# Optimization experiments

Hardware: AMD Instinct MI355X
Metric: run time of the kernel (lower is better)

Reference implementation:

```python
import jax, jax.numpy as jnp
import numpy as np

NUM_MODES = 13   # 8192x8192 weight, mode_base=2, z-order-grouped pairs -> 13 modes of size 4
RANK = 8
MODE = 4
NUM_BASIS = 32
OUT_F = 8192
IN_F = 8192


def setup_inputs() -> dict:
    key = jax.random.key(0)
    k1, k2, k3 = jax.random.split(key, 3)
    basis_weights = jnp.clip(jax.random.normal(k1, (NUM_MODES, NUM_BASIS), jnp.float32), -3.0, 3.0)
    basis = jax.random.normal(k2, (NUM_BASIS, RANK, MODE, RANK), jnp.float32)
    rank_adapters = jax.random.uniform(k3, (NUM_MODES, RANK), jnp.float32, 0.5, 1.5)
    return {"basis_weights": basis_weights, "basis": basis, "rank_adapters": rank_adapters}


def _chain(cores):
    # cores: list of (r, m, r) tensors; returns chained (r, m^len, r)
    T = cores[0]
    for G in cores[1:]:
        T = jnp.einsum('aib,bjc->aijc', T, G).reshape(RANK, -1, RANK)
    return T


def reference(basis_weights, basis, rank_adapters):
    # decompress_cores: small GEMM over the shared basis, then rank-adapter scaling ('linear' act)
    cores = (basis_weights @ basis.reshape(NUM_BASIS, -1)).reshape(NUM_MODES, RANK, MODE, RANK)
    cores = cores * rank_adapters[:, :, None, None]
    core_list = [cores[m] for m in range(NUM_MODES)]
    # tensor-ring contraction with trace; split chain in half to bound intermediate memory
    half = NUM_MODES // 2
    L = _chain(core_list[:half])    # (r, MODE^6, r)
    R = _chain(core_list[half:])    # (r, MODE^7, r)
    w = jnp.einsum('aib,bja->ij', L, R).reshape((MODE,) * NUM_MODES)
    # inverse z-order reshape: each mode-4 dim = (row-bit, col-bit) interleaved pair
    w = w.reshape((2,) * (2 * NUM_MODES))
    perm = tuple(range(0, 2 * NUM_MODES, 2)) + tuple(range(1, 2 * NUM_MODES, 2))
    w = jnp.transpose(w, perm).reshape(OUT_F, IN_F)
    return w
```

## Files before the change

### kernel.cpp

```cpp
#include <hip/hip_runtime.h>


using bf16x8 = __attribute__((ext_vector_type(8))) short;
using f32x4  = __attribute__((ext_vector_type(4))) float;
using f32x16 = __attribute__((ext_vector_type(16))) float;

#define WS_LA    4096
#define WS_LB    20480
#define WS_RA    24576
#define WS_RB    40960
#define BOFF_AHI 262144
#define BOFF_ALO 786432
#define BOFF_BHI 1310720
#define BOFF_BLO 3407872

__device__ __forceinline__ unsigned short f2bf(float x) {
    unsigned int u = __builtin_bit_cast(unsigned int, x);
    u += 0x7fffu + ((u >> 16) & 1u);
    return (unsigned short)(u >> 16);
}
__device__ __forceinline__ float bf2f(unsigned short b) {
    unsigned int u = ((unsigned int)b) << 16;
    return __builtin_bit_cast(float, u);
}

__global__ void k_chains(const float* __restrict__ bw,
                         const float* __restrict__ basis,
                         const float* __restrict__ ra,
                         float* __restrict__ ws) {
    __shared__ float sCores[13 * 256];
    __shared__ float buf0[4096];
    __shared__ float buf1[4096];
    const int tid   = threadIdx.x;
    const int chain = blockIdx.x;

    const int s0   = (chain == 0) ? 0 : (chain == 1) ? 4 : (chain == 2) ? 6 : 10;
    const int nm   = (chain == 0) ? 4 : (chain == 1) ? 2 : (chain == 2) ? 4 : 3;
    const int wout = (chain == 0) ? WS_LA : (chain == 1) ? WS_LB
                   : (chain == 2) ? WS_RA : WS_RB;

    for (int e = tid; e < 13 * 256; e += 256) {
        int m    = e >> 8;
        int r1   = (e >> 5) & 7;
        int rest = e & 255;
        float s = 0.f;
#pragma unroll
        for (int n = 0; n < 32; ++n)
            s = fmaf(bw[m * 32 + n], basis[n * 256 + rest], s);
        sCores[e] = s * ra[m * 8 + r1];
    }
    __syncthreads();

    const float* src = &sCores[s0 * 256];
    int mcurlog = 2;
    float* dst = buf0;
    for (int step = 1; step < nm; ++step) {
        const float* core = &sCores[(s0 + step) * 256];
        const int moutlog = mcurlog + 2;
        const int mout    = 1 << moutlog;
        const int total   = 64 << moutlog;
        const bool last   = (step == nm - 1);
        for (int e = tid; e < total; e += 256) {
            int b  = e & 7;
            int im = (e >> 3) & (mout - 1);
            int a  = e >> (3 + moutlog);
            int i  = im >> 2, mm = im & 3;
            float s = 0.f;
#pragma unroll
            for (int c = 0; c < 8; ++c)
                s = fmaf(src[((a << mcurlog) + i) * 8 + c],
                         core[(c * 4 + mm) * 8 + b], s);
            if (last) ws[wout + e] = s;
            else      dst[e]       = s;
        }
        __syncthreads();
        src = dst;
        dst = (dst == buf0) ? buf1 : buf0;
        mcurlog = moutlog;
    }
}

__device__ __forceinline__ int ilv(int r, int c, int nb) {
    int v = 0;
    for (int t = 0; t < nb; ++t)
        v |= (((c >> t) & 1) << (2 * t)) | (((r >> t) & 1) << (2 * t + 1));
    return v;
}

__global__ void k_build(float* __restrict__ ws) {
    int e = blockIdx.x * 256 + threadIdx.x;
    const float* LA = ws + WS_LA;
    const float* LB = ws + WS_LB;
    const float* RA = ws + WS_RA;
    const float* RB = ws + WS_RB;
    char* wsb = (char*)ws;
    unsigned short* Ahi = (unsigned short*)(wsb + BOFF_AHI);
    unsigned short* Alo = (unsigned short*)(wsb + BOFF_ALO);
    unsigned short* Bhi = (unsigned short*)(wsb + BOFF_BHI);
    unsigned short* Blo = (unsigned short*)(wsb + BOFF_BLO);

    if (e < 262144) {
        int k = e & 63, ch = (e >> 6) & 63, rh = e >> 12;
        int i  = ilv(rh, ch, 6);
        int iA = i >> 4, iB = i & 15;
        int a = k >> 3, b = k & 7;
        float s = 0.f;
#pragma unroll
        for (int c = 0; c < 8; ++c)
            s = fmaf(LA[(a * 256 + iA) * 8 + c], LB[(c * 16 + iB) * 8 + b], s);
        unsigned short h = f2bf(s);
        Ahi[e] = h;
        Alo[e] = f2bf(s - bf2f(h));
    } else {
        int idx = e - 262144;
        int k = idx & 63, n = idx >> 6;
        int rl = n >> 7, cl = n & 127;
        int j  = ilv(rl, cl, 7);
        int jA = j >> 6, jB = j & 63;
        int a = k >> 3, b = k & 7;
        float s = 0.f;
#pragma unroll
        for (int c = 0; c < 8; ++c)
            s = fmaf(RA[(b * 256 + jA) * 8 + c], RB[(c * 64 + jB) * 8 + a], s);
        unsigned short h = f2bf(s);
        Bhi[idx] = h;
        Blo[idx] = f2bf(s - bf2f(h));
    }
}

__global__ __launch_bounds__(256, 3) void k_out3(const float* __restrict__ ws,
                                                 float* __restrict__ out) {
    const char* wsb = (const char*)ws;
    const unsigned short* Ahi = (const unsigned short*)(wsb + BOFF_AHI);
    const unsigned short* Alo = (const unsigned short*)(wsb + BOFF_ALO);
    const unsigned short* Bhi = (const unsigned short*)(wsb + BOFF_BHI);
    const unsigned short* Blo = (const unsigned short*)(wsb + BOFF_BLO);

    const int tid  = threadIdx.x;
    const int lane = tid & 63;
    const int w    = tid >> 6;
    const int mb   = blockIdx.x >> 5;
    const int nbb  = blockIdx.x & 31;
    const int l31  = lane & 31;
    const int hi   = lane >> 5;

    bf16x8 Af0h[4], Af0l[4], Af1h[4], Af1l[4];
    {
        const int m0 = mb * 64 + l31;
        const int m1 = m0 + 32;
#pragma unroll
        for (int kk = 0; kk < 4; ++kk) {
            const int o = kk * 16 + hi * 8;
            Af0h[kk] = *(const bf16x8*)(Ahi + m0 * 64 + o);
            Af0l[kk] = *(const bf16x8*)(Alo + m0 * 64 + o);
            Af1h[kk] = *(const bf16x8*)(Ahi + m1 * 64 + o);
            Af1l[kk] = *(const bf16x8*)(Alo + m1 * 64 + o);
        }
    }

#pragma unroll 1
    for (int i = 0; i < 4; ++i) {
        const int nt = i * 4 + w;
        const int n0 = nbb * 512 + nt * 32;
        const int nrow = n0 + l31;

        bf16x8 Bfh[4], Bfl[4];
#pragma unroll
        for (int kk = 0; kk < 4; ++kk) {
            const int o = kk * 16 + hi * 8;
            Bfh[kk] = *(const bf16x8*)(Bhi + nrow * 64 + o);
            Bfl[kk] = *(const bf16x8*)(Blo + nrow * 64 + o);
        }

        f32x16 acc0 = {0,0,0,0,0,0,0,0,0,0,0,0,0,0,0,0};
        f32x16 acc1 = {0,0,0,0,0,0,0,0,0,0,0,0,0,0,0,0};
#pragma unroll
        for (int kk = 0; kk < 4; ++kk) {
            acc0 = __builtin_amdgcn_mfma_f32_32x32x16_bf16(Af0h[kk], Bfh[kk], acc0, 0, 0, 0);
            acc1 = __builtin_amdgcn_mfma_f32_32x32x16_bf16(Af1h[kk], Bfh[kk], acc1, 0, 0, 0);
            acc0 = __builtin_amdgcn_mfma_f32_32x32x16_bf16(Af0h[kk], Bfl[kk], acc0, 0, 0, 0);
            acc1 = __builtin_amdgcn_mfma_f32_32x32x16_bf16(Af1h[kk], Bfl[kk], acc1, 0, 0, 0);
            acc0 = __builtin_amdgcn_mfma_f32_32x32x16_bf16(Af0l[kk], Bfh[kk], acc0, 0, 0, 0);
            acc1 = __builtin_amdgcn_mfma_f32_32x32x16_bf16(Af1l[kk], Bfh[kk], acc1, 0, 0, 0);
        }

        const int rl  = n0 >> 7;
        const int clb = n0 & 127;
        float* __restrict__ obase =
            out + (((size_t)(mb * 128 + rl)) << 13) + clb + l31 + (size_t)hi * 512;
#pragma unroll
        for (int r = 0; r < 16; ++r) {
            const int drow = (r & 3) + 8 * (r >> 2);
            obase[(size_t)drow * 128]        = acc0[r];
            obase[(size_t)(drow + 32) * 128] = acc1[r];
        }
    }
}

extern "C" void kernel_launch(void* const* d_in, const int* in_sizes, int n_in,
                              void* d_out, int out_size, void* d_ws, size_t ws_size,
                              hipStream_t stream) {
    const float* bw    = (const float*)d_in[0];
    const float* basis = (const float*)d_in[1];
    const float* ra    = (const float*)d_in[2];
    float* out = (float*)d_out;
    float* ws  = (float*)d_ws;

    k_chains<<<4,    256, 0, stream>>>(bw, basis, ra, ws);
    k_build <<<5120, 256, 0, stream>>>(ws);
    k_out3  <<<2048, 256, 0, stream>>>(ws, out);
}
```

Measured before the change: 90.94 us.

## Split chain work across blocks, vectorize build, halve output tile per block

k_chains now runs 16 blocks per chain. Each block recomputes the earlier steps and writes only its own slice of the final step, which spreads the serial tail across more CUs. k_build has each thread compute 8 outputs, reusing loaded rows, and writes them as vector stores of hi/lo bf16 pairs, with 8x fewer threads. k_out now computes a 32-row tile per block instead of 64 and launches twice as many blocks with a higher occupancy hint. This trades some A-fragment reuse for more parallelism and less register pressure.

```diff
diff --git a/kernel.cpp b/kernel.cpp
--- a/kernel.cpp
+++ b/kernel.cpp
@@ -2,6 +2,7 @@
 
 
 using bf16x8 = __attribute__((ext_vector_type(8))) short;
+using u16x8  = __attribute__((ext_vector_type(8))) unsigned short;
 using f32x4  = __attribute__((ext_vector_type(4))) float;
 using f32x16 = __attribute__((ext_vector_type(16))) float;
 
@@ -32,7 +33,8 @@
     __shared__ float buf0[4096];
     __shared__ float buf1[4096];
     const int tid   = threadIdx.x;
-    const int chain = blockIdx.x;
+    const int chain = blockIdx.x >> 4;
+    const int slice = blockIdx.x & 15;
 
     const int s0   = (chain == 0) ? 0 : (chain == 1) ? 4 : (chain == 2) ? 6 : 10;
     const int nm   = (chain == 0) ? 4 : (chain == 1) ? 2 : (chain == 2) ? 4 : 3;
@@ -60,7 +62,10 @@
         const int mout    = 1 << moutlog;
         const int total   = 64 << moutlog;
         const bool last   = (step == nm - 1);
-        for (int e = tid; e < total; e += 256) {
+        const int sz   = total >> 4;
+        const int ebeg = last ? slice * sz : 0;
+        const int eend = last ? ebeg + sz  : total;
+        for (int e = ebeg + tid; e < eend; e += 256) {
             int b  = e & 7;
             int im = (e >> 3) & (mout - 1);
             int a  = e >> (3 + moutlog);
@@ -88,7 +93,7 @@
 }
 
 __global__ void k_build(float* __restrict__ ws) {
-    int e = blockIdx.x * 256 + threadIdx.x;
+    int idx = blockIdx.x * 256 + threadIdx.x;
     const float* LA = ws + WS_LA;
     const float* LB = ws + WS_LB;
     const float* RA = ws + WS_RA;
@@ -99,36 +104,64 @@
     unsigned short* Bhi = (unsigned short*)(wsb + BOFF_BHI);
     unsigned short* Blo = (unsigned short*)(wsb + BOFF_BLO);
 
-    if (e < 262144) {
-        int k = e & 63, ch = (e >> 6) & 63, rh = e >> 12;
+    float s[8];
+    unsigned short* ph;
+    unsigned short* pl;
+
+    if (idx < 32768) {
+        int a = idx & 7, m = idx >> 3;
+        int ch = m & 63, rh = m >> 6;
         int i  = ilv(rh, ch, 6);
         int iA = i >> 4, iB = i & 15;
-        int a = k >> 3, b = k & 7;
-        float s = 0.f;
-#pragma unroll
-        for (int c = 0; c < 8; ++c)
-            s = fmaf(LA[(a * 256 + iA) * 8 + c], LB[(c * 16 + iB) * 8 + b], s);
-        unsigned short h = f2bf(s);
-        Ahi[e] = h;
-        Alo[e] = f2bf(s - bf2f(h));
+        const float* lap = LA + (a * 256 + iA) * 8;
+        float la[8];
+#pragma unroll
+        for (int c = 0; c < 8; ++c) la[c] = lap[c];
+#pragma unroll
+        for (int b = 0; b < 8; ++b) s[b] = 0.f;
+#pragma unroll
+        for (int c = 0; c < 8; ++c) {
+            const float* lbp = LB + (c * 16 + iB) * 8;
+#pragma unroll
+            for (int b = 0; b < 8; ++b)
+                s[b] = fmaf(la[c], lbp[b], s[b]);
+        }
+        ph = Ahi + m * 64 + a * 8;
+        pl = Alo + m * 64 + a * 8;
     } else {
-        int idx = e - 262144;
-        int k = idx & 63, n = idx >> 6;
+        int t = idx - 32768;
+        int a = t & 7, n = t >> 3;
         int rl = n >> 7, cl = n & 127;
         int j  = ilv(rl, cl, 7);
         int jA = j >> 6, jB = j & 63;
-        int a = k >> 3, b = k & 7;
-        float s = 0.f;
-#pragma unroll
-        for (int c = 0; c < 8; ++c)
-            s = fmaf(RA[(b * 256 + jA) * 8 + c], RB[(c * 64 + jB) * 8 + a], s);
-        unsigned short h = f2bf(s);
-        Bhi[idx] = h;
-        Blo[idx] = f2bf(s - bf2f(h));
-    }
-}
-
-__global__ __launch_bounds__(256, 3) void k_out3(const float* __restrict__ ws,
+        float rb[8];
+#pragma unroll
+        for (int c = 0; c < 8; ++c) rb[c] = RB[(c * 64 + jB) * 8 + a];
+#pragma unroll
+        for (int b = 0; b < 8; ++b) {
+            const float* rap = RA + (b * 256 + jA) * 8;
+            float acc = 0.f;
+#pragma unroll
+            for (int c = 0; c < 8; ++c)
+                acc = fmaf(rap[c], rb[c], acc);
+            s[b] = acc;
+        }
+        ph = Bhi + n * 64 + a * 8;
+        pl = Blo + n * 64 + a * 8;
+    }
+
+    u16x8 vh, vl;
+#pragma unroll
+    for (int b = 0; b < 8; ++b) {
+        unsigned short h = f2bf(s[b]);
+        vh[b] = h;
+        vl[b] = f2bf(s[b] - bf2f(h));
+    }
+    *(u16x8*)ph = vh;
+    *(u16x8*)pl = vl;
+}
+
+__global__ __launch_bounds__(256, 4) void k_out4(const float* __restrict__ ws,
                                                  float* __restrict__ out) {
     const char* wsb = (const char*)ws;
     const unsigned short* Ahi = (const unsigned short*)(wsb + BOFF_AHI);
@@ -139,24 +172,24 @@
     const int tid  = threadIdx.x;
     const int lane = tid & 63;
     const int w    = tid >> 6;
-    const int mb   = blockIdx.x >> 5;
+    const int mb2  = blockIdx.x >> 5;
     const int nbb  = blockIdx.x & 31;
     const int l31  = lane & 31;
     const int hi   = lane >> 5;
 
-    bf16x8 Af0h[4], Af0l[4], Af1h[4], Af1l[4];
+    bf16x8 Afh[4], Afl[4];
     {
-        const int m0 = mb * 64 + l31;
-        const int m1 = m0 + 32;
+        const int m0 = mb2 * 32 + l31;
 #pragma unroll
         for (int kk = 0; kk < 4; ++kk) {
             const int o = kk * 16 + hi * 8;
-            Af0h[kk] = *(const bf16x8*)(Ahi + m0 * 64 + o);
-            Af0l[kk] = *(const bf16x8*)(Alo + m0 * 64 + o);
-            Af1h[kk] = *(const bf16x8*)(Ahi + m1 * 64 + o);
-            Af1l[kk] = *(const bf16x8*)(Alo + m1 * 64 + o);
-        }
-    }
+            Afh[kk] = *(const bf16x8*)(Ahi + m0 * 64 + o);
+            Afl[kk] = *(const bf16x8*)(Alo + m0 * 64 + o);
+        }
+    }
+
+    const size_t rowb = ((size_t)(mb2 >> 1)) << 20;
+    const int    colb = (mb2 & 1) << 12;
 
 #pragma unroll 1
     for (int i = 0; i < 4; ++i) {
@@ -172,27 +205,22 @@
             Bfl[kk] = *(const bf16x8*)(Blo + nrow * 64 + o);
         }
 
-        f32x16 acc0 = {0,0,0,0,0,0,0,0,0,0,0,0,0,0,0,0};
-        f32x16 acc1 = {0,0,0,0,0,0,0,0,0,0,0,0,0,0,0,0};
+        f32x16 acc = {0,0,0,0,0,0,0,0,0,0,0,0,0,0,0,0};
 #pragma unroll
         for (int kk = 0; kk < 4; ++kk) {
-            acc0 = __builtin_amdgcn_mfma_f32_32x32x16_bf16(Af0h[kk], Bfh[kk], acc0, 0, 0, 0);
-            acc1 = __builtin_amdgcn_mfma_f32_32x32x16_bf16(Af1h[kk], Bfh[kk], acc1, 0, 0, 0);
-            acc0 = __builtin_amdgcn_mfma_f32_32x32x16_bf16(Af0h[kk], Bfl[kk], acc0, 0, 0, 0);
-            acc1 = __builtin_amdgcn_mfma_f32_32x32x16_bf16(Af1h[kk], Bfl[kk], acc1, 0, 0, 0);
-            acc0 = __builtin_amdgcn_mfma_f32_32x32x16_bf16(Af0l[kk], Bfh[kk], acc0, 0, 0, 0);
-            acc1 = __builtin_amdgcn_mfma_f32_32x32x16_bf16(Af1l[kk], Bfh[kk], acc1, 0, 0, 0);
+            acc = __builtin_amdgcn_mfma_f32_32x32x16_bf16(Afh[kk], Bfh[kk], acc, 0, 0, 0);
+            acc = __builtin_amdgcn_mfma_f32_32x32x16_bf16(Afh[kk], Bfl[kk], acc, 0, 0, 0);
+            acc = __builtin_amdgcn_mfma_f32_32x32x16_bf16(Afl[kk], Bfh[kk], acc, 0, 0, 0);
         }
 
         const int rl  = n0 >> 7;
         const int clb = n0 & 127;
         float* __restrict__ obase =
-            out + (((size_t)(mb * 128 + rl)) << 13) + clb + l31 + (size_t)hi * 512;
+            out + rowb + ((size_t)rl << 13) + colb + clb + l31 + (size_t)hi * 512;
 #pragma unroll
         for (int r = 0; r < 16; ++r) {
             const int drow = (r & 3) + 8 * (r >> 2);
-            obase[(size_t)drow * 128]        = acc0[r];
-            obase[(size_t)(drow + 32) * 128] = acc1[r];
+            obase[(size_t)drow * 128] = acc[r];
         }
     }
 }
@@ -206,7 +234,7 @@
     float* out = (float*)d_out;
     float* ws  = (float*)d_ws;
 
-    k_chains<<<4,    256, 0, stream>>>(bw, basis, ra, ws);
-    k_build <<<5120, 256, 0, stream>>>(ws);
-    k_out3  <<<2048, 256, 0, stream>>>(ws, out);
-}
+    k_chains<<<64,  256, 0, stream>>>(bw, basis, ra, ws);
+    k_build <<<640, 256, 0, stream>>>(ws);
+    k_out4  <<<4096, 256, 0, stream>>>(ws, out);
+}
```

New measurement: 107.3 us. 1.18x slower.
